# Optimization experiments

Hardware: AMD Instinct MI355X
Metric: run time of the kernel (lower is better)

## Reference

```python
import jax, jax.numpy as jnp
import numpy as np

N = 2900000
B = 4096
D = 768
GAMMA = 0.8
EPS = 1e-14
TAU_MIN, TAU_MAX = 0.005, 0.05
RHO = 8.0
ETA_INIT = 0.03
BETA_U = 0.5
GRAD_CLIP = 5.0
TAU_INIT = 0.01


def setup_inputs() -> dict:
    key = jax.random.key(0)
    k1, k2, k3, k4, k5, k6 = jax.random.split(key, 6)
    img = jax.random.normal(k1, (B, D), jnp.float32)
    img = img / jnp.linalg.norm(img, axis=-1, keepdims=True)  # CLIP-style unit-norm embeddings
    txt = jax.random.normal(k2, (B, D), jnp.float32)
    txt = txt / jnp.linalg.norm(txt, axis=-1, keepdims=True)
    image_ids = jax.random.randint(k3, (B,), 0, N, dtype=jnp.int32)
    text_ids = jax.random.randint(k4, (B,), 0, N, dtype=jnp.int32)
    return {
        "image_features": img,
        "text_features": txt,
        "image_ids": image_ids,
        "text_ids": text_ids,
        "epoch": 1,
        "max_epoch": 30,
        "s_I": jax.random.uniform(k5, (N,), jnp.float32),
        "s_T": jax.random.uniform(k6, (N,), jnp.float32),
        "b_I": jnp.zeros((N,), jnp.float32),
        "b_T": jnp.zeros((N,), jnp.float32),
        "u_I": jnp.zeros((N,), jnp.float32),
        "u_T": jnp.zeros((N,), jnp.float32),
        "tau_I": jnp.full((N,), TAU_INIT, jnp.float32),
        "tau_T": jnp.full((N,), TAU_INIT, jnp.float32),
    }


def reference(image_features, text_features, image_ids, text_ids, epoch, max_epoch,
              s_I, s_T, b_I, b_T, u_I, u_T, tau_I, tau_T):
    sim = jnp.einsum("id,jd->ij", image_features, text_features)  # [B, B]
    diag_sim = jnp.diagonal(sim)
    bsz = sim.shape[0]
    mask_neg = 1.0 - jnp.eye(bsz, dtype=sim.dtype)

    tau_image = tau_I[image_ids]  # [B]
    tau_text = tau_T[text_ids]    # [B]

    image_diffs = sim - diag_sim[:, None]
    text_diffs = sim - diag_sim[None, :]
    # torch .detach() -> stop_gradient; everything downstream of these is detached too
    idt = jax.lax.stop_gradient(image_diffs / tau_image[:, None])
    tdt = jax.lax.stop_gradient(text_diffs / tau_text[None, :])

    old_b_I = b_I[image_ids]
    new_b_I = jnp.maximum(jnp.max(idt, axis=1), old_b_I)  # running row-max
    old_b_T = b_T[text_ids]
    new_b_T = jnp.maximum(jnp.max(tdt, axis=0), old_b_T)  # running col-max

    exp_i = jnp.exp(idt - new_b_I[:, None]) * mask_neg
    exp_t = jnp.exp(tdt - new_b_T[None, :]) * mask_neg
    g_I = jnp.sum(exp_i, axis=1)  # [B]
    g_T = jnp.sum(exp_t, axis=0)  # [B]

    if epoch == 0:
        sI = g_I
        sT = g_T
    else:
        sI = (1.0 - GAMMA) * s_I[image_ids] * jnp.exp(old_b_I - new_b_I) + GAMMA * g_I
        sT = (1.0 - GAMMA) * s_T[text_ids] * jnp.exp(old_b_T - new_b_T) + GAMMA * g_T

    sI_c = jnp.maximum(sI, EPS)
    sT_c = jnp.maximum(sT, EPS)

    w_i = exp_i / sI_c[:, None]
    w_t = exp_t / sT_c[None, :]

    image_loss = jnp.sum(w_i * image_diffs, axis=1)  # [B]
    text_loss = jnp.sum(w_t * text_diffs, axis=0)    # [B]
    total_loss = image_loss.mean() + text_loss.mean()

    twi = jnp.log(sI_c / (bsz - 1)) + new_b_I + RHO - jnp.sum(w_i * idt, axis=1)
    twt = jnp.log(sT_c / (bsz - 1)) + new_b_T + RHO - jnp.sum(w_t * tdt, axis=0)

    u_I_b = (1.0 - BETA_U) * u_I[image_ids] + BETA_U * jnp.clip(twi, -GRAD_CLIP, GRAD_CLIP)
    u_T_b = (1.0 - BETA_U) * u_T[text_ids] + BETA_U * jnp.clip(twt, -GRAD_CLIP, GRAD_CLIP)
    tau_I_b = jnp.clip(tau_image - ETA_INIT * u_I_b, TAU_MIN, TAU_MAX)
    tau_T_b = jnp.clip(tau_text - ETA_INIT * u_T_b, TAU_MIN, TAU_MAX)

    # torch mutates the persistent buffers in place; expose the updates as outputs
    b_I_new = b_I.at[image_ids].set(new_b_I)
    b_T_new = b_T.at[text_ids].set(new_b_T)
    s_I_new = s_I.at[image_ids].set(sI)
    s_T_new = s_T.at[text_ids].set(sT)
    u_I_new = u_I.at[image_ids].set(u_I_b)
    u_T_new = u_T.at[text_ids].set(u_T_b)
    tau_I_new = tau_I.at[image_ids].set(tau_I_b)
    tau_T_new = tau_T.at[text_ids].set(tau_T_b)

    return (total_loss, tau_image, tau_text,
            s_I_new, s_T_new, b_I_new, b_T_new, u_I_new, u_T_new, tau_I_new, tau_T_new)
```

## Files before the change

### kernel.cpp

```cpp
#include <hip/hip_runtime.h>
#include <hip/hip_bf16.h>
#include <math.h>

#define N_ITEMS 2900000
#define BDIM 4096
#define DDIM 768

typedef float f32x4 __attribute__((ext_vector_type(4)));
typedef __bf16 bf16x8 __attribute__((ext_vector_type(8)));

__device__ inline unsigned short f2bf(float f) {
    unsigned int u = __float_as_uint(f);
    unsigned int lsb = (u >> 16) & 1u;
    u += 0x7fffu + lsb;
    return (unsigned short)(u >> 16);
}

__device__ inline void gload16(const void* g, void* l) {
    __builtin_amdgcn_global_load_lds(
        (const __attribute__((address_space(1))) void*)g,
        (__attribute__((address_space(3))) void*)l, 16, 0, 0);
}

__global__ __launch_bounds__(256) void prep_kernel(
        const float* __restrict__ img, const float* __restrict__ txt,
        const int* __restrict__ image_ids, const int* __restrict__ text_ids,
        const float* __restrict__ tau_I, const float* __restrict__ tau_T,
        unsigned short* __restrict__ Xbf, unsigned short* __restrict__ Ybf,
        float* __restrict__ diag, float* __restrict__ tau_row,
        float* __restrict__ out) {
    const int bx = blockIdx.x;
    if (bx < 1536) {
        const int per = (BDIM * DDIM) / 4;
        for (int u = bx * 256 + threadIdx.x; u < 2 * per; u += 1536 * 256) {
            const float4* src = (u < per) ? (const float4*)img : (const float4*)txt;
            unsigned short* dst = (u < per) ? Xbf : Ybf;
            int i = (u < per) ? u : u - per;
            float4 v = src[i];
            ushort4 o;
            o.x = f2bf(v.x); o.y = f2bf(v.y); o.z = f2bf(v.z); o.w = f2bf(v.w);
            ((ushort4*)dst)[i] = o;
        }
        return;
    }
    const int w = (bx - 1536) * 4 + (threadIdx.x >> 6);
    const int lane = threadIdx.x & 63;
    const float* a = img + (size_t)w * DDIM;
    const float* b = txt + (size_t)w * DDIM;
    float s = 0.f;
    for (int d = lane; d < DDIM; d += 64) s += a[d] * b[d];
    #pragma unroll
    for (int d = 32; d >= 1; d >>= 1) s += __shfl_xor(s, d);
    if (lane == 0) diag[w] = s;
    if (lane == 1) {
        float t = tau_I[image_ids[w]];
        tau_row[w] = t;
        out[1 + w] = t;
    }
    if (lane == 2) {
        float t = tau_T[text_ids[w]];
        tau_row[BDIM + w] = t;
        out[1 + BDIM + w] = t;
    }
}

__global__ __launch_bounds__(256) void copy_kernel(
        const float* s0, const float* s1, const float* s2, const float* s3,
        const float* s4, const float* s5, const float* s6, const float* s7,
        float* dst) {
    const int n4 = N_ITEMS / 4;
    #pragma unroll
    for (int k = 0; k < 8; k++) {
        const float* s;
        switch (k) {
            case 0: s = s0; break; case 1: s = s1; break;
            case 2: s = s2; break; case 3: s = s3; break;
            case 4: s = s4; break; case 5: s = s5; break;
            case 6: s = s6; break; default: s = s7; break;
        }
        float* d = dst + (size_t)k * N_ITEMS;
        for (int i = blockIdx.x * 256 + threadIdx.x; i < n4; i += 2048 * 256) {
            float4 v = ((const float4*)s)[i];
            float* dd = d + (size_t)i * 4;
            dd[0] = v.x; dd[1] = v.y; dd[2] = v.z; dd[3] = v.w;
        }
    }
}

__global__ __launch_bounds__(512) void gemm_kernel(
        const unsigned short* __restrict__ Xbf, const unsigned short* __restrict__ Ybf,
        const float* __restrict__ diag, const float* __restrict__ tau_row,
        float* __restrict__ partials ) {
    __shared__ unsigned short As[2][16384];
    __shared__ unsigned short Bs[2][16384];

    const int cb = blockIdx.x, rb = blockIdx.y;
    const int t = threadIdx.x;
    const int wave = t >> 6, lane = t & 63;
    const int wr = wave >> 2, wc = wave & 3;
    const int g = lane >> 4, r16 = lane & 15;

    f32x4 acc[8][4];
    #pragma unroll
    for (int m = 0; m < 8; m++)
        #pragma unroll
        for (int n = 0; n < 4; n++)
            #pragma unroll
            for (int q = 0; q < 4; q++) acc[m][n][q] = 0.f;

    const int srow = t >> 3;
    const int sgr  = (t & 7) ^ (srow & 7);
    const unsigned short* pA[4];
    const unsigned short* pB[4];
    #pragma unroll
    for (int i = 0; i < 4; i++) {
        pA[i] = Xbf + (size_t)(rb * 256 + i * 64 + srow) * DDIM + sgr * 8;
        pB[i] = Ybf + (size_t)(cb * 256 + i * 64 + srow) * DDIM + sgr * 8;
    }

    #define STAGE(buf, kk) do {                                                   \
        const size_t ko_ = (size_t)(kk) * 64;                                     \
        _Pragma("unroll")                                                         \
        for (int i_ = 0; i_ < 4; i_++) {                                          \
            gload16(pA[i_] + ko_, (char*)As + (buf)*32768 + i_*8192 + wave*1024); \
            gload16(pB[i_] + ko_, (char*)Bs + (buf)*32768 + i_*8192 + wave*1024); \
        }                                                                         \
    } while (0)

    STAGE(0, 0);
    __syncthreads();

    int cur = 0;
    for (int kk = 0; kk < 12; ++kk) {
        if (kk < 11) STAGE(cur ^ 1, kk + 1);
        const char* Ac = (const char*)As + cur * 32768;
        const char* Bc = (const char*)Bs + cur * 32768;
        #pragma unroll
        for (int ks = 0; ks < 2; ++ks) {
            bf16x8 af[8], bfr[4];
            #pragma unroll
            for (int m = 0; m < 8; m++) {
                const int row = wr * 128 + m * 16 + r16;
                const int gr = (ks * 4 + g) ^ (r16 & 7);
                af[m] = *(const bf16x8*)(Ac + row * 128 + gr * 16);
            }
            #pragma unroll
            for (int n = 0; n < 4; n++) {
                const int row = wc * 64 + n * 16 + r16;
                const int gr = (ks * 4 + g) ^ (r16 & 7);
                bfr[n] = *(const bf16x8*)(Bc + row * 128 + gr * 16);
            }
            #pragma unroll
            for (int m = 0; m < 8; m++)
                #pragma unroll
                for (int n = 0; n < 4; n++)
                    acc[m][n] = __builtin_amdgcn_mfma_f32_16x16x32_bf16(af[m], bfr[n], acc[m][n], 0, 0, 0);
        }
        __syncthreads();
        cur ^= 1;
    }
    #undef STAGE

    const int R0 = rb * 256 + wr * 128;
    const int C0 = cb * 256 + wc * 64;

    #pragma unroll
    for (int m = 0; m < 8; m++) {
        #pragma unroll
        for (int q = 0; q < 4; q++) {
            const int rowg = R0 + m * 16 + g * 4 + q;
            const float dgv = diag[rowg];
            const float itau = 1.0f / tau_row[rowg];
            float x4[4];
            float mloc = -3.0e38f;
            #pragma unroll
            for (int n = 0; n < 4; n++) {
                const int colg = C0 + n * 16 + r16;
                const float x = (acc[m][n][q] - dgv) * itau;
                x4[n] = x;
                mloc = (colg != rowg) ? fmaxf(mloc, x) : mloc;
            }
            #pragma unroll
            for (int d = 1; d < 16; d <<= 1) mloc = fmaxf(mloc, __shfl_xor(mloc, d));
            float E = 0.f, F = 0.f;
            #pragma unroll
            for (int n = 0; n < 4; n++) {
                const int colg = C0 + n * 16 + r16;
                const float e = (colg != rowg) ? __expf(x4[n] - mloc) : 0.f;
                E += e; F += e * x4[n];
            }
            #pragma unroll
            for (int d = 1; d < 16; d <<= 1) {
                E += __shfl_xor(E, d);
                F += __shfl_xor(F, d);
            }
            if (r16 == 0) {
                const int chunk = cb * 4 + wc;
                float* pp = partials + (((size_t)rowg) * 64 + chunk) * 3;
                pp[0] = mloc; pp[1] = E; pp[2] = F;
            }
        }
    }

    #pragma unroll
    for (int n = 0; n < 4; n++) {
        const int colg = C0 + n * 16 + r16;
        const float dgc = diag[colg];
        const float itc = 1.0f / tau_row[BDIM + colg];
        float mloc = -3.0e38f;
        #pragma unroll
        for (int m = 0; m < 8; m++)
            #pragma unroll
            for (int q = 0; q < 4; q++) {
                const int rowg = R0 + m * 16 + g * 4 + q;
                const float x = (acc[m][n][q] - dgc) * itc;
                mloc = (rowg != colg) ? fmaxf(mloc, x) : mloc;
            }
        mloc = fmaxf(mloc, __shfl_xor(mloc, 16));
        mloc = fmaxf(mloc, __shfl_xor(mloc, 32));
        float E = 0.f, F = 0.f;
        #pragma unroll
        for (int m = 0; m < 8; m++)
            #pragma unroll
            for (int q = 0; q < 4; q++) {
                const int rowg = R0 + m * 16 + g * 4 + q;
                const float x = (acc[m][n][q] - dgc) * itc;
                const float e = (rowg != colg) ? __expf(x - mloc) : 0.f;
                E += e; F += e * x;
            }
        E += __shfl_xor(E, 16); F += __shfl_xor(F, 16);
        E += __shfl_xor(E, 32); F += __shfl_xor(F, 32);
        if (g == 0) {
            const int rchunk = rb * 2 + wr;
            float* pp = partials + (((size_t)BDIM + colg) * 64 + rchunk) * 3;
            pp[0] = mloc; pp[1] = E; pp[2] = F;
        }
    }
}

__global__ __launch_bounds__(256) void tail_kernel(
        const float* __restrict__ partials,
        const int* __restrict__ image_ids, const int* __restrict__ text_ids,
        const float* __restrict__ b_I, const float* __restrict__ b_T,
        const float* __restrict__ s_I, const float* __restrict__ s_T,
        const float* __restrict__ u_I, const float* __restrict__ u_T,
        const float* __restrict__ tau_row, const int* __restrict__ epoch_ptr,
        float* __restrict__ loss_arr, float* __restrict__ out) {
    __shared__ int sids[BDIM];
    const int bx = blockIdx.x;
    const int p = bx >> 10;
    const int* ids = p ? text_ids : image_ids;
    for (int i = threadIdx.x; i < BDIM / 4; i += 256)
        ((int4*)sids)[i] = ((const int4*)ids)[i];

    const int wave = threadIdx.x >> 6, lane = threadIdx.x & 63;
    const int row = (bx & 1023) * 4 + wave;
    float m, E, F;
    if (p == 1 && lane >= 32) {
        m = -3.0e38f; E = 0.f; F = 0.f;
    } else {
        const float* pp = partials + (((size_t)p * BDIM + row) * 64 + lane) * 3;
        m = pp[0]; E = pp[1]; F = pp[2];
    }
    #pragma unroll
    for (int d = 1; d < 64; d <<= 1) {
        float mo = __shfl_xor(m, d), Eo = __shfl_xor(E, d), Fo = __shfl_xor(F, d);
        float mn = fmaxf(m, mo);
        float a1 = expf(m - mn), a2 = expf(mo - mn);
        E = E * a1 + Eo * a2;
        F = F * a1 + Fo * a2;
        m = mn;
    }
    const int id = ids[row];
    const float ob = p ? b_T[id] : b_I[id];
    const float so = p ? s_T[id] : s_I[id];
    const float uo = p ? u_T[id] : u_I[id];
    const float tv = tau_row[p * BDIM + row];
    const float m0 = fmaxf(ob, 0.0f);
    if (m0 > m) { float sc = expf(m - m0); E *= sc; F *= sc; m = m0; }
    float sI = (*epoch_ptr == 0) ? E : 0.2f * so * expf(ob - m) + 0.8f * E;
    float sc_ = fmaxf(sI, 1e-14f);
    float ratio = F / sc_;
    float twi = logf(sc_ * (1.0f / 4095.0f)) + m + 8.0f - ratio;
    float uc = fminf(fmaxf(twi, -5.0f), 5.0f);
    float ub = 0.5f * uo + 0.5f * uc;
    float tb = fminf(fmaxf(tv - 0.03f * ub, 0.005f), 0.05f);
    if (lane == 0) loss_arr[p * BDIM + row] = tv * ratio;

    __syncthreads();
    const int myid = sids[row];
    bool dup = false;
    for (int c = row + 1 + lane; c < BDIM; c += 64)
        dup |= (sids[c] == myid);
    if (__any(dup)) return;
    if (lane < 4) {
        const float v = (lane == 0) ? m : (lane == 1) ? sI : (lane == 2) ? ub : tb;
        const int arr = (lane == 0) ? (2 + p) : (lane == 1) ? (0 + p)
                      : (lane == 2) ? (4 + p) : (6 + p);
        out[8193 + (size_t)arr * N_ITEMS + myid] = v;
    }
}

__global__ void loss_kernel(const float* __restrict__ loss_arr, float* __restrict__ out) {
    __shared__ float wsum[16];
    int t = threadIdx.x;
    float s = 0.f;
    for (int i = t; i < 2 * BDIM; i += 1024) s += loss_arr[i];
    #pragma unroll
    for (int d = 32; d >= 1; d >>= 1) s += __shfl_xor(s, d);
    if ((t & 63) == 0) wsum[t >> 6] = s;
    __syncthreads();
    if (t == 0) {
        float tot = 0.f;
        for (int i = 0; i < 16; i++) tot += wsum[i];
        out[0] = tot * (1.0f / (float)BDIM);
    }
}

extern "C" void kernel_launch(void* const* d_in, const int* in_sizes, int n_in,
                              void* d_out, int out_size, void* d_ws, size_t ws_size,
                              hipStream_t stream) {
    const float* img       = (const float*)d_in[0];
    const float* txt       = (const float*)d_in[1];
    const int*   image_ids = (const int*)d_in[2];
    const int*   text_ids  = (const int*)d_in[3];
    const int*   epoch     = (const int*)d_in[4];
    const float* s_I   = (const float*)d_in[6];
    const float* s_T   = (const float*)d_in[7];
    const float* b_I   = (const float*)d_in[8];
    const float* b_T   = (const float*)d_in[9];
    const float* u_I   = (const float*)d_in[10];
    const float* u_T   = (const float*)d_in[11];
    const float* tau_I = (const float*)d_in[12];
    const float* tau_T = (const float*)d_in[13];
    float* out = (float*)d_out;

    char* ws = (char*)d_ws;
    unsigned short* Xbf = (unsigned short*)ws;
    unsigned short* Ybf = (unsigned short*)(ws + 6291456);
    float* diag     = (float*)(ws + 12582912);
    float* tau_row  = (float*)(ws + 12599296);
    float* partials = (float*)(ws + 12632064);
    float* loss_arr = (float*)(ws + 18923520);

    prep_kernel<<<2560, 256, 0, stream>>>(img, txt, image_ids, text_ids, tau_I, tau_T,
                                          Xbf, Ybf, diag, tau_row, out);
    gemm_kernel<<<dim3(16, 16), 512, 0, stream>>>(Xbf, Ybf, diag, tau_row, partials);
    copy_kernel<<<2048, 256, 0, stream>>>(s_I, s_T, b_I, b_T, u_I, u_T, tau_I, tau_T,
                                          out + 8193);
    tail_kernel<<<2048, 256, 0, stream>>>(partials, image_ids, text_ids,
                                          b_I, b_T, s_I, s_T, u_I, u_T,
                                          tau_row, epoch, loss_arr, out);
    loss_kernel<<<1, 1024, 0, stream>>>(loss_arr, out);
}
```

Before: 109.3 us.

## Fuse bulk state copy into GEMM main loop to overlap memory traffic with MFMA

Removes the separate copy kernel that duplicates the eight N-length state arrays into the output, and spreads that copy across the GEMM's K-loop iterations. Each GEMM thread loads float4 chunks with nontemporal loads and stores them a stage later, so the memory-bound copy can overlap with matrix compute. The cost is extra registers and memory-pipe pressure inside the GEMM, which can lower occupancy or slow the LDS staging loads.

```diff
diff --git a/kernel.cpp b/kernel.cpp
--- a/kernel.cpp
+++ b/kernel.cpp
@@ -64,33 +64,13 @@
     }
 }
 
-__global__ __launch_bounds__(256) void copy_kernel(
-        const float* s0, const float* s1, const float* s2, const float* s3,
-        const float* s4, const float* s5, const float* s6, const float* s7,
-        float* dst) {
-    const int n4 = N_ITEMS / 4;
-    #pragma unroll
-    for (int k = 0; k < 8; k++) {
-        const float* s;
-        switch (k) {
-            case 0: s = s0; break; case 1: s = s1; break;
-            case 2: s = s2; break; case 3: s = s3; break;
-            case 4: s = s4; break; case 5: s = s5; break;
-            case 6: s = s6; break; default: s = s7; break;
-        }
-        float* d = dst + (size_t)k * N_ITEMS;
-        for (int i = blockIdx.x * 256 + threadIdx.x; i < n4; i += 2048 * 256) {
-            float4 v = ((const float4*)s)[i];
-            float* dd = d + (size_t)i * 4;
-            dd[0] = v.x; dd[1] = v.y; dd[2] = v.z; dd[3] = v.w;
-        }
-    }
-}
-
 __global__ __launch_bounds__(512) void gemm_kernel(
         const unsigned short* __restrict__ Xbf, const unsigned short* __restrict__ Ybf,
         const float* __restrict__ diag, const float* __restrict__ tau_row,
-        float* __restrict__ partials ) {
+        float* __restrict__ partials ,
+        const float* s0, const float* s1, const float* s2, const float* s3,
+        const float* s4, const float* s5, const float* s6, const float* s7,
+        float* __restrict__ cdst ) {
     __shared__ unsigned short As[2][16384];
     __shared__ unsigned short Bs[2][16384];
 
@@ -127,12 +107,50 @@
         }                                                                         \
     } while (0)
 
+    const int gtid = (rb * 16 + cb) * 512 + t;
+    f32x4 cval[4];
+    int cu_[4];
+    auto srcp = [&](int k) -> const float* {
+        switch (k) {
+            case 0: return s0; case 1: return s1; case 2: return s2; case 3: return s3;
+            case 4: return s4; case 5: return s5; case 6: return s6; default: return s7;
+        }
+    };
+    auto CLOAD = [&](int slot, int c) {
+        const int u = c * 131072 + gtid;
+        cu_[slot] = u;
+        if (u < 5800000) {
+            const int k = u / 725000;
+            const int i = u - k * 725000;
+            cval[slot] = __builtin_nontemporal_load((const f32x4*)srcp(k) + i);
+        }
+    };
+    auto CSTORE = [&](int slot) {
+        const int u = cu_[slot];
+        if (u < 5800000) {
+            const int k = u / 725000;
+            const int i = u - k * 725000;
+            float* dd = cdst + (size_t)k * N_ITEMS + (size_t)i * 4;
+            __builtin_nontemporal_store(cval[slot][0], dd + 0);
+            __builtin_nontemporal_store(cval[slot][1], dd + 1);
+            __builtin_nontemporal_store(cval[slot][2], dd + 2);
+            __builtin_nontemporal_store(cval[slot][3], dd + 3);
+        }
+    };
+
     STAGE(0, 0);
+    #pragma unroll
+    for (int j = 0; j < 4; j++) CLOAD(j, j);
     __syncthreads();
 
     int cur = 0;
     for (int kk = 0; kk < 12; ++kk) {
         if (kk < 11) STAGE(cur ^ 1, kk + 1);
+        #pragma unroll
+        for (int j = 0; j < 4; j++) {
+            CSTORE(j);
+            if (kk < 11) CLOAD(j, (kk + 1) * 4 + j);
+        }
         const char* Ac = (const char*)As + cur * 32768;
         const char* Bc = (const char*)Bs + cur * 32768;
         #pragma unroll
@@ -345,9 +363,9 @@
 
     prep_kernel<<<2560, 256, 0, stream>>>(img, txt, image_ids, text_ids, tau_I, tau_T,
                                           Xbf, Ybf, diag, tau_row, out);
-    gemm_kernel<<<dim3(16, 16), 512, 0, stream>>>(Xbf, Ybf, diag, tau_row, partials);
-    copy_kernel<<<2048, 256, 0, stream>>>(s_I, s_T, b_I, b_T, u_I, u_T, tau_I, tau_T,
-                                          out + 8193);
+    gemm_kernel<<<dim3(16, 16), 512, 0, stream>>>(Xbf, Ybf, diag, tau_row, partials,
+                                                  s_I, s_T, b_I, b_T, u_I, u_T,
+                                                  tau_I, tau_T, out + 8193);
     tail_kernel<<<2048, 256, 0, stream>>>(partials, image_ids, text_ids,
                                           b_I, b_T, s_I, s_T, u_I, u_T,
                                           tau_row, epoch, loss_arr, out);
```

Result: faster. 104.4 us (-4.5%).
